# Kernel optimization log

Measured on AMD Instinct MI355X. Metric: run time of the kernel, lower is better.

The kernel has to match this reference:

```python
import jax, jax.numpy as jnp
import numpy as np

B, N, D, H, M = 4, 1024, 768, 12, 100
HD = D // H
FF = 4 * D


def layer_norm(x, g, b, eps=1e-5):
    mu = x.mean(-1, keepdims=True)
    var = ((x - mu) ** 2).mean(-1, keepdims=True)
    return (x - mu) / jnp.sqrt(var + eps) * g + b


def _rel_pos_logits(q_pos, rel_emb):
    """Fairseq LearnedRelativePositionalEmbedding (unmasked, per-head).
    q_pos: (B, N, H, HD). Faithful to the torch call: flat reshape to (N, B*H, HD).
    Returns absolute-indexed positional logits of shape (B*H, N, N)."""
    b, l, h, d = q_pos.shape
    query = q_pos.reshape(l, b * h, d)  # flat reshape exactly as in torch code
    pad_len = max(l - M, 0)
    start = max(M - l, 0)
    emb = rel_emb[..., 0]  # (H, 2M-1, HD)
    emb = jnp.pad(emb, ((0, 0), (pad_len, pad_len), (0, 0)))
    emb = jax.lax.dynamic_slice_in_dim(emb, start, 2 * l - 1, axis=1)
    emb = jax.lax.stop_gradient(emb)  # torch wraps the pad in no_grad
    qv = query.reshape(l, -1, h, d)  # (l, B, H, HD)
    pl = jnp.einsum('lbhd,hmd->lbhm', qv, emb).reshape(l, -1, 2 * l - 1)
    if pad_len > 0:  # mask relative positions beyond max_relative_pos
        mask = np.zeros((2 * l - 1,), np.float32)
        mask[:pad_len] = -1e8
        mask[2 * l - 1 - pad_len:] = -1e8
        pl = pl + jnp.asarray(mask)
    # relative -> absolute indexing (unmasked skewing trick)
    xp = jnp.pad(pl, ((0, 0), (0, 0), (0, 1)))          # (l, BH, 2l)
    xp = xp.transpose(1, 0, 2).reshape(b * h, l * 2 * l)
    xp = jnp.pad(xp, ((0, 0), (0, l - 1)))
    xp = xp.reshape(b * h, l + 1, 2 * l - 1)
    return xp[:, :l, l - 1:]                             # (BH, l, l)


def setup_inputs() -> dict:
    key = jax.random.key(0)
    ks = jax.random.split(key, 8)
    p = lambda k, shape: jax.random.normal(k, shape, dtype=jnp.float32) * 0.02
    return {
        'src': jax.random.normal(ks[0], (B, N, D), dtype=jnp.float32),
        'qkv_w': p(ks[1], (3 * D, D)),
        'qkv_b': jnp.zeros((3 * D,), jnp.float32),
        'rel_emb': jax.random.normal(ks[2], (H, 2 * M - 1, HD, 1), dtype=jnp.float32) * (HD ** -0.5),
        'proj_w': p(ks[3], (D, D)),
        'proj_b': jnp.zeros((D,), jnp.float32),
        'ln1_g': jnp.ones((D,), jnp.float32),
        'ln1_b': jnp.zeros((D,), jnp.float32),
        'fc1_w': p(ks[4], (FF, D)),
        'fc1_b': jnp.zeros((FF,), jnp.float32),
        'fc2_w': p(ks[5], (D, FF)),
        'fc2_b': jnp.zeros((D,), jnp.float32),
        'ln2_g': jnp.ones((D,), jnp.float32),
        'ln2_b': jnp.zeros((D,), jnp.float32),
    }


def reference(src, qkv_w, qkv_b, rel_emb, proj_w, proj_b, ln1_g, ln1_b,
              fc1_w, fc1_b, fc2_w, fc2_b, ln2_g, ln2_b):
    b, n, dmod = src.shape
    qkv = (src @ qkv_w.T + qkv_b).reshape(b, n, 3, H, HD).transpose(2, 0, 3, 1, 4)
    q, k, v = qkv[0], qkv[1], qkv[2]  # (B, H, N, HD)
    logits = jnp.einsum('bhnd,bhmd->bhnm', q, k) * (1.0 / np.sqrt(HD))
    pos = _rel_pos_logits(q.transpose(0, 2, 1, 3), rel_emb).reshape(b, H, n, n)
    probs = jax.nn.softmax(logits + pos, axis=-1)  # dropout is identity at eval / p=0
    out = jnp.einsum('bhnm,bhmd->bhnd', probs, v).transpose(0, 2, 1, 3).reshape(b, n, dmod)
    attn_out = out @ proj_w.T + proj_b
    x = layer_norm(src + attn_out, ln1_g, ln1_b)
    h1 = jax.nn.gelu(x @ fc1_w.T + fc1_b, approximate=False)
    x = layer_norm(x + h1 @ fc2_w.T + fc2_b, ln2_g, ln2_b)
    return x
```

## Files before the change

### kernel.cpp

```cpp
#include <hip/hip_runtime.h>
#include <hip/hip_bf16.h>
#include <math.h>


typedef __attribute__((ext_vector_type(8))) short bf16x8;
typedef __attribute__((ext_vector_type(4))) float f32x4;

#define GLDS16(g, l) __builtin_amdgcn_global_load_lds( \
    (const __attribute__((address_space(1))) void*)(g), \
    (__attribute__((address_space(3))) void*)(l), 16, 0, 0)

__device__ __forceinline__ unsigned short f2bu(float x) {
    union { __hip_bfloat16 h; unsigned short u; } c;
    c.h = __float2bfloat16(x);
    return c.u;
}
__device__ __forceinline__ float bu2f(unsigned short u) {
    union { __hip_bfloat16 h; unsigned short u; } c;
    c.u = u;
    return __bfloat162float(c.h);
}

__global__ void __launch_bounds__(256)
convert_all_kernel(const float* __restrict__ s0, const float* __restrict__ s1,
                   const float* __restrict__ s2, const float* __restrict__ s3,
                   const float* __restrict__ s4,
                   unsigned short* __restrict__ d0, unsigned short* __restrict__ d1,
                   unsigned short* __restrict__ d2, unsigned short* __restrict__ d3,
                   unsigned short* __restrict__ d4)
{
    const int idx = blockIdx.x * 256 + threadIdx.x;
    const float* s; unsigned short* d; int off;
    if (idx < 786432)       { s = s0; d = d0; off = idx; }
    else if (idx < 1228800) { s = s1; d = d1; off = idx - 786432; }
    else if (idx < 1376256) { s = s2; d = d2; off = idx - 1228800; }
    else if (idx < 1966080) { s = s3; d = d3; off = idx - 1376256; }
    else if (idx < 2555904) { s = s4; d = d4; off = idx - 1966080; }
    else return;
    const float4 v = ((const float4*)s)[off];
    ushort4 o;
    o.x = f2bu(v.x); o.y = f2bu(v.y); o.z = f2bu(v.z); o.w = f2bu(v.w);
    ((ushort4*)d)[off] = o;
}

__global__ void __launch_bounds__(256)
embpad_kernel(const float* __restrict__ rel, unsigned short* __restrict__ embpad)
{
    const int idx = blockIdx.x * 256 + threadIdx.x;
    if (idx >= 12 * 256 * 64) return;
    const int d = idx & 63;
    const int rp = (idx >> 6) & 255;
    const int h = idx >> 14;
    embpad[idx] = (rp < 199) ? f2bu(rel[((h * 199 + rp) << 6) + d]) : (unsigned short)0;
}

#define SWZ_OFF(ch, row7) ((((ch) ^ (row7)) * 8))

template<int MODE>
__global__ void __launch_bounds__(256)
gemm64_kernel(const unsigned short* __restrict__ A, const unsigned short* __restrict__ Wt,
              const float* __restrict__ bias, unsigned short* __restrict__ Cb,
              int Ndim, int K, int Ksplit,
              unsigned short* __restrict__ qb, unsigned short* __restrict__ kb,
              unsigned short* __restrict__ vTb)
{
    __shared__ short As[2 * 128 * 64];
    __shared__ short Bs[2 * 64 * 64];
    const int tid = threadIdx.x;
    const int l = tid & 63;
    const int w = tid >> 6;
    const int wr = w >> 1, wc = w & 1;

    int flat = blockIdx.y * gridDim.x + blockIdx.x;
    const int nxy = gridDim.x * gridDim.y;
    flat = (flat & 7) * (nxy >> 3) + (flat >> 3);
    const int bx = flat % gridDim.x;
    const int by = flat / gridDim.x;

    const int row0 = by * 128;
    const int col0 = bx * 64;
    const int koff = blockIdx.z * Ksplit;
    const int nt = Ksplit >> 6;

    const int lrow = l >> 3;
    const int lcol = ((l & 7) ^ lrow) * 8;
    const int l7 = l & 7;

    f32x4 acc[4][2];
#pragma unroll
    for (int m = 0; m < 4; ++m)
#pragma unroll
        for (int n = 0; n < 2; ++n) acc[m][n] = (f32x4){0.f, 0.f, 0.f, 0.f};

#define STAGE(buf, t) do {                                                        \
    const int k0 = koff + (t) * 64;                                               \
    _Pragma("unroll")                                                             \
    for (int it = 0; it < 4; ++it) {                                              \
        const int c = w * 4 + it;                                                 \
        GLDS16(A + (size_t)(row0 + c * 8 + lrow) * K + k0 + lcol,                 \
               As + (buf) * 8192 + c * 512);                                      \
    }                                                                             \
    _Pragma("unroll")                                                             \
    for (int it = 0; it < 2; ++it) {                                              \
        const int c = w * 2 + it;                                                 \
        GLDS16(Wt + (size_t)(col0 + c * 8 + lrow) * K + k0 + lcol,                \
               Bs + (buf) * 4096 + c * 512);                                      \
    }                                                                             \
} while (0)

    STAGE(0, 0);

    for (int t = 0; t < nt; ++t) {
        const int buf = t & 1;
        if (t + 1 < nt) {
            STAGE(buf ^ 1, t + 1);
            asm volatile("s_waitcnt vmcnt(6)" ::: "memory");
        } else {
            asm volatile("s_waitcnt vmcnt(0)" ::: "memory");
        }
        __builtin_amdgcn_sched_barrier(0);
        __builtin_amdgcn_s_barrier();

        const short* a = As + buf * 8192;
        const short* bsp = Bs + buf * 4096;
        __builtin_amdgcn_s_setprio(1);
#pragma unroll
        for (int kk = 0; kk < 2; ++kk) {
            const int ch = kk * 4 + (l >> 4);
            bf16x8 af[4], bfr[2];
#pragma unroll
            for (int m = 0; m < 4; ++m)
                af[m] = *(const bf16x8*)(a + (wr * 64 + m * 16 + (l & 15)) * 64 + SWZ_OFF(ch, l7));
#pragma unroll
            for (int n = 0; n < 2; ++n)
                bfr[n] = *(const bf16x8*)(bsp + (wc * 32 + n * 16 + (l & 15)) * 64 + SWZ_OFF(ch, l7));
#pragma unroll
            for (int m = 0; m < 4; ++m)
#pragma unroll
                for (int n = 0; n < 2; ++n)
                    acc[m][n] = __builtin_amdgcn_mfma_f32_16x16x32_bf16(af[m], bfr[n], acc[m][n], 0, 0, 0);
        }
        __builtin_amdgcn_s_setprio(0);
        if (t + 1 < nt)
            __builtin_amdgcn_s_barrier();
    }
#undef STAGE

#pragma unroll
    for (int m = 0; m < 4; ++m) {
#pragma unroll
        for (int n = 0; n < 2; ++n) {
#pragma unroll
            for (int r = 0; r < 4; ++r) {
                const int row = row0 + wr * 64 + m * 16 + (l >> 4) * 4 + r;
                const int col = col0 + wc * 32 + n * 16 + (l & 15);
                if (MODE == 0) {
                    const float v = acc[m][n][r] + bias[col];
                    const int which = col / 768;
                    const int rem = col - which * 768;
                    const int h = rem >> 6, d = rem & 63;
                    const int b = row >> 10, nn = row & 1023;
                    if (which == 0)
                        qb[((size_t)(b * 12 + h) * 1024 + nn) * 64 + d] = f2bu(v);
                    else if (which == 1)
                        kb[((size_t)(b * 12 + h) * 1024 + nn) * 64 + d] = f2bu(v);
                    else
                        vTb[((size_t)(b * 12 + h) * 64 + d) * 1024 + nn] = f2bu(v);
                } else if (MODE == 2) {
                    const float v = acc[m][n][r] + bias[col];
                    const float u = 0.7978845608028654f * (v + 0.044715f * v * v * v);
                    const float th = 1.0f - 2.0f / (__expf(2.0f * u) + 1.0f);
                    Cb[(size_t)row * Ndim + col] = f2bu(0.5f * v * (1.0f + th));
                } else {
                    unsigned short* dst = Cb + (size_t)blockIdx.z * 4096 * Ndim;
                    dst[(size_t)row * Ndim + col] = f2bu(acc[m][n][r]);
                }
            }
        }
    }
}

__global__ void __launch_bounds__(256)
attn_mfma_kernel(const unsigned short* __restrict__ qb, const unsigned short* __restrict__ kb,
                 const unsigned short* __restrict__ vTb, const unsigned short* __restrict__ embpad,
                 unsigned short* __restrict__ ctx)
{
    __shared__ __attribute__((aligned(16))) char lds[58368];
    short* Qps = (short*)(lds);
    short* Qs = (short*)(lds);
    short* Stage = (short*)(lds + 8192);
    unsigned short* Spos = (unsigned short*)(lds + 24576);
    short* PLall = (short*)(lds);
    short* Vt = (short*)(lds + 40960);

    const int i0 = blockIdx.x * 64;
    const int h = blockIdx.y, b = blockIdx.z;
    const int tid = threadIdx.x;
    const int l = tid & 63, w = tid >> 6;
    const int lm = l & 15, lg4 = l >> 4;
    const int l7 = l & 7;
    const int lrow = l >> 3;
    const int lcolsw = ((l & 7) ^ lrow) * 8;
    const size_t bh = (size_t)(b * 12 + h);

#pragma unroll
    for (int c = 0; c < 2; ++c) {
        const int row = w * 16 + c * 8 + lrow;
        const int iq = i0 + row;
        const int t2 = iq * 4 + b;
        const int b2 = t2 >> 10, n2 = t2 & 1023;
        const unsigned short* g = qb + ((size_t)(b2 * 12 + h) * 1024 + n2) * 64 + lcolsw;
        GLDS16(g, Qps + (w * 16 + c * 8) * 64);
    }
    __syncthreads();

    bf16x8 afp[2];
#pragma unroll
    for (int kk = 0; kk < 2; ++kk)
        afp[kk] = *(const bf16x8*)(Qps + (w * 16 + lm) * 64 + SWZ_OFF(kk * 4 + lg4, l7));

#pragma unroll
    for (int et = 0; et < 4; ++et) {
        __syncthreads();
#pragma unroll
        for (int c = 0; c < 2; ++c) {
            const int row = w * 16 + c * 8 + lrow;
            const unsigned short* g = embpad + ((size_t)h * 256 + et * 64 + row) * 64 + lcolsw;
            GLDS16(g, Stage + (w * 16 + c * 8) * 64);
        }
        __syncthreads();
        f32x4 cp[4];
#pragma unroll
        for (int sub = 0; sub < 4; ++sub) cp[sub] = (f32x4){0.f, 0.f, 0.f, 0.f};
#pragma unroll
        for (int kk = 0; kk < 2; ++kk)
#pragma unroll
            for (int sub = 0; sub < 4; ++sub) {
                const bf16x8 bv = *(const bf16x8*)(Stage + (sub * 16 + lm) * 64 + SWZ_OFF(kk * 4 + lg4, l7));
                cp[sub] = __builtin_amdgcn_mfma_f32_16x16x32_bf16(afp[kk], bv, cp[sub], 0, 0, 0);
            }
#pragma unroll
        for (int sub = 0; sub < 4; ++sub)
#pragma unroll
            for (int r = 0; r < 4; ++r)
                Spos[(w * 16 + lg4 * 4 + r) * 264 + et * 64 + sub * 16 + lm] = f2bu(cp[sub][r]);
    }

#pragma unroll
    for (int c = 0; c < 2; ++c) {
        const int row = w * 16 + c * 8 + lrow;
        const unsigned short* g = qb + (bh * 1024 + i0 + row) * 64 + lcolsw;
        GLDS16(g, Qs + (w * 16 + c * 8) * 64);
    }

    const int jw0 = (i0 > 128) ? i0 - 128 : 0;
    const int hiex = (i0 + 163 < 1024) ? i0 + 163 : 1024;
    const int nt = (hiex - jw0 + 63) >> 6;

    f32x4 s[5][4];
#pragma unroll
    for (int ct = 0; ct < 5; ++ct)
#pragma unroll
        for (int sub = 0; sub < 4; ++sub) s[ct][sub] = (f32x4){0.f, 0.f, 0.f, 0.f};
    bf16x8 afq[2];

#pragma unroll
    for (int ct = 0; ct < 5; ++ct) {
        __syncthreads();
        if (ct < nt) {
#pragma unroll
            for (int c = 0; c < 2; ++c) {
                const int row = w * 16 + c * 8 + lrow;
                const unsigned short* g = kb + (bh * 1024 + jw0 + ct * 64 + row) * 64 + lcolsw;
                GLDS16(g, Stage + (w * 16 + c * 8) * 64);
            }
        }
        __syncthreads();
        if (ct == 0) {
#pragma unroll
            for (int kk = 0; kk < 2; ++kk)
                afq[kk] = *(const bf16x8*)(Qs + (w * 16 + lm) * 64 + SWZ_OFF(kk * 4 + lg4, l7));
        }
        if (ct < nt) {
#pragma unroll
            for (int kk = 0; kk < 2; ++kk)
#pragma unroll
                for (int sub = 0; sub < 4; ++sub) {
                    const bf16x8 bv = *(const bf16x8*)(Stage + (sub * 16 + lm) * 64 + SWZ_OFF(kk * 4 + lg4, l7));
                    s[ct][sub] = __builtin_amdgcn_mfma_f32_16x16x32_bf16(afq[kk], bv, s[ct][sub], 0, 0, 0);
                }
        }
    }

    const int irel = w * 16 + lg4 * 4;
    float mx[4] = {-1e30f, -1e30f, -1e30f, -1e30f};
#pragma unroll
    for (int ct = 0; ct < 5; ++ct)
#pragma unroll
        for (int sub = 0; sub < 4; ++sub)
#pragma unroll
            for (int r = 0; r < 4; ++r) {
                const int i = i0 + irel + r;
                const int j = jw0 + ct * 64 + sub * 16 + lm;
                const int rr = j - i + 99;
                const int rc = (rr < 0) ? 0 : (rr > 198 ? 198 : rr);
                const float ps = bu2f(Spos[(irel + r) * 264 + rc]);
                const bool ok = (ct < nt) && (rr >= 0) && (rr <= 198);
                const float lg = ok ? (0.125f * s[ct][sub][r] + ps) : -1e30f;
                s[ct][sub][r] = lg;
                mx[r] = fmaxf(mx[r], lg);
            }
#pragma unroll
    for (int m = 1; m < 16; m <<= 1)
#pragma unroll
        for (int r = 0; r < 4; ++r) mx[r] = fmaxf(mx[r], __shfl_xor(mx[r], m, 64));

    float sm[4] = {0.f, 0.f, 0.f, 0.f};
#pragma unroll
    for (int ct = 0; ct < 5; ++ct)
#pragma unroll
        for (int sub = 0; sub < 4; ++sub)
#pragma unroll
            for (int r = 0; r < 4; ++r) {
                const float p = __expf(s[ct][sub][r] - mx[r]);
                s[ct][sub][r] = p;
                sm[r] += p;
            }
#pragma unroll
    for (int m = 1; m < 16; m <<= 1)
#pragma unroll
        for (int r = 0; r < 4; ++r) sm[r] += __shfl_xor(sm[r], m, 64);
    float inv[4];
#pragma unroll
    for (int r = 0; r < 4; ++r) inv[r] = 1.0f / sm[r];

    __syncthreads();

    short* PLw = PLall + w * 5120;
#pragma unroll
    for (int ct = 0; ct < 5; ++ct)
#pragma unroll
        for (int sub = 0; sub < 4; ++sub)
#pragma unroll
            for (int r = 0; r < 4; ++r) {
                const int rowrel = lg4 * 4 + r;
                const int colrel = ct * 64 + sub * 16 + lm;
                int byte = rowrel * 640 + colrel * 2;
                byte ^= ((rowrel & 7) << 4);
                *(short*)((char*)PLw + byte) = (short)f2bu(s[ct][sub][r] * inv[r]);
            }

    f32x4 o[4];
#pragma unroll
    for (int sub = 0; sub < 4; ++sub) o[sub] = (f32x4){0.f, 0.f, 0.f, 0.f};
#pragma unroll
    for (int ct = 0; ct < 5; ++ct) {
        if (ct < nt) {
#pragma unroll
            for (int c = 0; c < 2; ++c) {
                const int dd = w * 16 + c * 8 + lrow;
                const unsigned short* g = vTb + (bh * 64 + dd) * 1024 + jw0 + ct * 64 + lcolsw;
                GLDS16(g, Vt + (w * 16 + c * 8) * 64);
            }
        }
        __syncthreads();
        if (ct < nt) {
#pragma unroll
            for (int kk = 0; kk < 2; ++kk) {
                const int colrel = ct * 64 + kk * 32 + lg4 * 8;
                int byte = lm * 640 + colrel * 2;
                byte ^= ((lm & 7) << 4);
                const bf16x8 ap = *(const bf16x8*)((char*)PLw + byte);
#pragma unroll
                for (int sub = 0; sub < 4; ++sub) {
                    const bf16x8 bv = *(const bf16x8*)(Vt + (sub * 16 + lm) * 64 + SWZ_OFF(kk * 4 + lg4, l7));
                    o[sub] = __builtin_amdgcn_mfma_f32_16x16x32_bf16(ap, bv, o[sub], 0, 0, 0);
                }
            }
        }
        __syncthreads();
    }

#pragma unroll
    for (int sub = 0; sub < 4; ++sub)
#pragma unroll
        for (int r = 0; r < 4; ++r) {
            const int i = i0 + w * 16 + lg4 * 4 + r;
            const int d = sub * 16 + lm;
            ctx[((size_t)b * 1024 + i) * 768 + h * 64 + d] = f2bu(o[sub][r]);
        }
}

__global__ void __launch_bounds__(256)
ln_fuse_kernel(const unsigned short* __restrict__ p0, const unsigned short* __restrict__ p1,
               const float* __restrict__ bias,
               const float* __restrict__ residf, const unsigned short* __restrict__ residb,
               const float* __restrict__ g, const float* __restrict__ bta,
               float* __restrict__ outf, unsigned short* __restrict__ outb)
{
    const int row = blockIdx.x;
    const int t = threadIdx.x;
    const size_t base = (size_t)row * 768;
    float v[3];
#pragma unroll
    for (int e = 0; e < 3; ++e) {
        const int idx = t + e * 256;
        const float r = residf ? residf[base + idx] : bu2f(residb[base + idx]);
        v[e] = bu2f(p0[base + idx]) + bu2f(p1[base + idx]) + bias[idx] + r;
    }
    __shared__ float red[4];
    float s = v[0] + v[1] + v[2];
#pragma unroll
    for (int off = 32; off > 0; off >>= 1) s += __shfl_down(s, off);
    if ((t & 63) == 0) red[t >> 6] = s;
    __syncthreads();
    const float mu = (red[0] + red[1] + red[2] + red[3]) * (1.0f / 768.0f);
    __syncthreads();
    const float d0 = v[0] - mu, d1 = v[1] - mu, d2 = v[2] - mu;
    float q = d0 * d0 + d1 * d1 + d2 * d2;
#pragma unroll
    for (int off = 32; off > 0; off >>= 1) q += __shfl_down(q, off);
    if ((t & 63) == 0) red[t >> 6] = q;
    __syncthreads();
    const float var = (red[0] + red[1] + red[2] + red[3]) * (1.0f / 768.0f);
    const float rstd = rsqrtf(var + 1e-5f);
    const float y0 = d0 * rstd * g[t] + bta[t];
    const float y1 = d1 * rstd * g[t + 256] + bta[t + 256];
    const float y2 = d2 * rstd * g[t + 512] + bta[t + 512];
    if (outf) { outf[base + t] = y0; outf[base + t + 256] = y1; outf[base + t + 512] = y2; }
    if (outb) { outb[base + t] = f2bu(y0); outb[base + t + 256] = f2bu(y1); outb[base + t + 512] = f2bu(y2); }
}

extern "C" void kernel_launch(void* const* d_in, const int* in_sizes, int n_in,
                              void* d_out, int out_size, void* d_ws, size_t ws_size,
                              hipStream_t stream)
{
    const float* src    = (const float*)d_in[0];
    const float* qkv_w  = (const float*)d_in[1];
    const float* qkv_b  = (const float*)d_in[2];
    const float* rel    = (const float*)d_in[3];
    const float* proj_w = (const float*)d_in[4];
    const float* proj_b = (const float*)d_in[5];
    const float* ln1_g  = (const float*)d_in[6];
    const float* ln1_b  = (const float*)d_in[7];
    const float* fc1_w  = (const float*)d_in[8];
    const float* fc1_b  = (const float*)d_in[9];
    const float* fc2_w  = (const float*)d_in[10];
    const float* fc2_b  = (const float*)d_in[11];
    const float* ln2_g  = (const float*)d_in[12];
    const float* ln2_b  = (const float*)d_in[13];
    float* out = (float*)d_out;
    char* W = (char*)d_ws;

    unsigned short* q_b     = (unsigned short*)(W + 0);
    unsigned short* k_b     = (unsigned short*)(W + 6291456);
    unsigned short* vT_b    = (unsigned short*)(W + 12582912);
    unsigned short* src_b   = (unsigned short*)(W + 18874368);
    unsigned short* ctx_b   = (unsigned short*)(W + 18874368);
    unsigned short* h1_b    = (unsigned short*)(W + 0);
    unsigned short* qkvw_b  = (unsigned short*)(W + 25165824);
    unsigned short* PP      = (unsigned short*)(W + 25165824);
    unsigned short* FP      = (unsigned short*)(W + 25165824);
    unsigned short* projw_b = (unsigned short*)(W + 37748736);
    unsigned short* fc1w_b  = (unsigned short*)(W + 38928384);
    unsigned short* fc2w_b  = (unsigned short*)(W + 43646976);
    unsigned short* embp_b  = (unsigned short*)(W + 48365568);
    unsigned short* xbuf_b  = (unsigned short*)(W + 48758784);

    convert_all_kernel<<<9984, 256, 0, stream>>>(
        src, qkv_w, proj_w, fc1_w, fc2_w, src_b, qkvw_b, projw_b, fc1w_b, fc2w_b);
    embpad_kernel<<<768, 256, 0, stream>>>(rel, embp_b);

    gemm64_kernel<0><<<dim3(36, 32, 1), 256, 0, stream>>>(
        src_b, qkvw_b, qkv_b, nullptr, 2304, 768, 768, q_b, k_b, vT_b);

    attn_mfma_kernel<<<dim3(16, 12, 4), 256, 0, stream>>>(q_b, k_b, vT_b, embp_b, ctx_b);

    gemm64_kernel<3><<<dim3(12, 32, 2), 256, 0, stream>>>(
        ctx_b, projw_b, nullptr, PP, 768, 768, 384, nullptr, nullptr, nullptr);

    ln_fuse_kernel<<<4096, 256, 0, stream>>>(
        PP, PP + 4096 * 768, proj_b, src, nullptr, ln1_g, ln1_b, nullptr, xbuf_b);

    gemm64_kernel<2><<<dim3(48, 32, 1), 256, 0, stream>>>(
        xbuf_b, fc1w_b, fc1_b, h1_b, 3072, 768, 768, nullptr, nullptr, nullptr);

    gemm64_kernel<3><<<dim3(12, 32, 2), 256, 0, stream>>>(
        h1_b, fc2w_b, nullptr, FP, 768, 3072, 1536, nullptr, nullptr, nullptr);

    ln_fuse_kernel<<<4096, 256, 0, stream>>>(
        FP, FP + 4096 * 768, fc2_b, nullptr, xbuf_b, ln2_g, ln2_b, out, nullptr);
}
```

Measured before the change: 170.9 us.

## Load GEMM B operand directly into registers instead of LDS staging

The GEMM kernel no longer stages weight tiles through shared memory. Each wave loads its B fragments straight from global memory into registers, double-buffered across a manually unrolled two-step k loop, and only A goes through LDS. This cuts LDS traffic and halves shared memory so that occupancy can rise, with a launch bound of 4 blocks/CU added. The trade-off is uncoalesced per-lane global loads of B that are duplicated across waves sharing columns, plus more register pressure. The loop also assumes nt is even.

```diff
diff --git a/kernel.cpp b/kernel.cpp
--- a/kernel.cpp
+++ b/kernel.cpp
@@ -57,7 +57,7 @@
 #define SWZ_OFF(ch, row7) ((((ch) ^ (row7)) * 8))
 
 template<int MODE>
-__global__ void __launch_bounds__(256)
+__global__ void __launch_bounds__(256, 4)
 gemm64_kernel(const unsigned short* __restrict__ A, const unsigned short* __restrict__ Wt,
               const float* __restrict__ bias, unsigned short* __restrict__ Cb,
               int Ndim, int K, int Ksplit,
@@ -65,7 +65,6 @@
               unsigned short* __restrict__ vTb)
 {
     __shared__ short As[2 * 128 * 64];
-    __shared__ short Bs[2 * 64 * 64];
     const int tid = threadIdx.x;
     const int l = tid & 63;
     const int w = tid >> 6;
@@ -85,6 +84,7 @@
     const int lrow = l >> 3;
     const int lcol = ((l & 7) ^ lrow) * 8;
     const int l7 = l & 7;
+    const int lm = l & 15, lg4 = l >> 4;
 
     f32x4 acc[4][2];
 #pragma unroll
@@ -92,7 +92,7 @@
 #pragma unroll
         for (int n = 0; n < 2; ++n) acc[m][n] = (f32x4){0.f, 0.f, 0.f, 0.f};
 
-#define STAGE(buf, t) do {                                                        \
+#define STAGEA(buf, t) do {                                                       \
     const int k0 = koff + (t) * 64;                                               \
     _Pragma("unroll")                                                             \
     for (int it = 0; it < 4; ++it) {                                              \
@@ -100,51 +100,67 @@
         GLDS16(A + (size_t)(row0 + c * 8 + lrow) * K + k0 + lcol,                 \
                As + (buf) * 8192 + c * 512);                                      \
     }                                                                             \
+} while (0)
+
+#define LOADB(dst, t) do {                                                        \
+    const int k0 = koff + (t) * 64;                                               \
     _Pragma("unroll")                                                             \
-    for (int it = 0; it < 2; ++it) {                                              \
-        const int c = w * 2 + it;                                                 \
-        GLDS16(Wt + (size_t)(col0 + c * 8 + lrow) * K + k0 + lcol,                \
-               Bs + (buf) * 4096 + c * 512);                                      \
+    for (int kk = 0; kk < 2; ++kk)                                                \
+        _Pragma("unroll")                                                         \
+        for (int n = 0; n < 2; ++n)                                               \
+            dst[kk][n] = *(const bf16x8*)(Wt +                                    \
+                (size_t)(col0 + wc * 32 + n * 16 + lm) * K + k0 + (kk * 4 + lg4) * 8); \
+} while (0)
+
+#define COMPUTE(buf, Bf) do {                                                     \
+    const short* a_ = As + (buf) * 8192;                                          \
+    _Pragma("unroll")                                                             \
+    for (int kk = 0; kk < 2; ++kk) {                                              \
+        const int ch = kk * 4 + lg4;                                              \
+        bf16x8 af[4];                                                             \
+        _Pragma("unroll")                                                         \
+        for (int m = 0; m < 4; ++m)                                               \
+            af[m] = *(const bf16x8*)(a_ + (wr * 64 + m * 16 + lm) * 64 + SWZ_OFF(ch, l7)); \
+        _Pragma("unroll")                                                         \
+        for (int m = 0; m < 4; ++m)                                               \
+            _Pragma("unroll")                                                     \
+            for (int n = 0; n < 2; ++n)                                           \
+                acc[m][n] = __builtin_amdgcn_mfma_f32_16x16x32_bf16(af[m], Bf[kk][n], acc[m][n], 0, 0, 0); \
     }                                                                             \
 } while (0)
 
-    STAGE(0, 0);
-
-    for (int t = 0; t < nt; ++t) {
-        const int buf = t & 1;
-        if (t + 1 < nt) {
-            STAGE(buf ^ 1, t + 1);
-            asm volatile("s_waitcnt vmcnt(6)" ::: "memory");
+    bf16x8 BfA[2][2], BfB[2][2];
+    STAGEA(0, 0);
+    LOADB(BfA, 0);
+
+    for (int t = 0; t < nt; t += 2) {
+        STAGEA(1, t + 1);
+        LOADB(BfB, t + 1);
+        asm volatile("s_waitcnt vmcnt(8)" ::: "memory");
+        __builtin_amdgcn_sched_barrier(0);
+        __builtin_amdgcn_s_barrier();
+        __builtin_amdgcn_s_setprio(1);
+        COMPUTE(0, BfA);
+        __builtin_amdgcn_s_setprio(0);
+        __builtin_amdgcn_s_barrier();
+
+        if (t + 2 < nt) {
+            STAGEA(0, t + 2);
+            LOADB(BfA, t + 2);
+            asm volatile("s_waitcnt vmcnt(8)" ::: "memory");
         } else {
             asm volatile("s_waitcnt vmcnt(0)" ::: "memory");
         }
         __builtin_amdgcn_sched_barrier(0);
         __builtin_amdgcn_s_barrier();
-
-        const short* a = As + buf * 8192;
-        const short* bsp = Bs + buf * 4096;
         __builtin_amdgcn_s_setprio(1);
-#pragma unroll
-        for (int kk = 0; kk < 2; ++kk) {
-            const int ch = kk * 4 + (l >> 4);
-            bf16x8 af[4], bfr[2];
-#pragma unroll
-            for (int m = 0; m < 4; ++m)
-                af[m] = *(const bf16x8*)(a + (wr * 64 + m * 16 + (l & 15)) * 64 + SWZ_OFF(ch, l7));
-#pragma unroll
-            for (int n = 0; n < 2; ++n)
-                bfr[n] = *(const bf16x8*)(bsp + (wc * 32 + n * 16 + (l & 15)) * 64 + SWZ_OFF(ch, l7));
-#pragma unroll
-            for (int m = 0; m < 4; ++m)
-#pragma unroll
-                for (int n = 0; n < 2; ++n)
-                    acc[m][n] = __builtin_amdgcn_mfma_f32_16x16x32_bf16(af[m], bfr[n], acc[m][n], 0, 0, 0);
-        }
+        COMPUTE(1, BfB);
         __builtin_amdgcn_s_setprio(0);
-        if (t + 1 < nt)
-            __builtin_amdgcn_s_barrier();
-    }
-#undef STAGE
+        if (t + 2 < nt) __builtin_amdgcn_s_barrier();
+    }
+#undef STAGEA
+#undef LOADB
+#undef COMPUTE
 
 #pragma unroll
     for (int m = 0; m < 4; ++m) {
```

Result: slower. 230.6 us (+34.9%).
